# Kernel optimization log

Hardware: AMD Instinct MI355X
Metric: run time of the kernel (lower is better)

## Reference

```python
import jax, jax.numpy as jnp
import numpy as np

D_STATE = 16
D_CONV = 4


def _ln_cf(x, w, b, eps=1e-6):
    # channels_first LayerNorm over dim 1 of (B,C,H,W)
    u = x.mean(1, keepdims=True)
    s = ((x - u) ** 2).mean(1, keepdims=True)
    return w[:, None, None] * ((x - u) / jnp.sqrt(s + eps)) + b[:, None, None]


def _ln_last(x, w, b, eps=1e-5):
    u = x.mean(-1, keepdims=True)
    s = ((x - u) ** 2).mean(-1, keepdims=True)
    return (x - u) / jnp.sqrt(s + eps) * w + b


def _mamba(xn, Win, convw, convb, Wx, Wdt, bdt, Alog, Dp):
    # xn: (B, L, d_model); returns (B, L, d_inner) (out_proj is Identity in this module)
    B, L, _ = xn.shape
    di = Win.shape[0] // 2
    xz = xn @ Win.T                                   # (B,L,2*di), in_proj bias=False
    xc, z = xz[..., :di], xz[..., di:]
    # causal depthwise conv1d along L (pad left d_conv-1, slice == torch pad+trim)
    xt = jnp.pad(xc.transpose(0, 2, 1), ((0, 0), (0, 0), (D_CONV - 1, 0)))
    xt = jax.lax.conv_general_dilated(xt, convw[:, None, :], (1,), 'VALID',
                                      dimension_numbers=('NCH', 'OIH', 'NCH'),
                                      feature_group_count=di)
    xs = jax.nn.silu(xt + convb[None, :, None]).transpose(0, 2, 1)  # (B,L,di)
    dtr = Wdt.shape[1]
    x_dbl = xs @ Wx.T                                 # (B,L,dtr+2*ds)
    dt = x_dbl[..., :dtr]
    Bm = x_dbl[..., dtr:dtr + D_STATE]                # (B,L,ds)
    Cm = x_dbl[..., dtr + D_STATE:]                   # (B,L,ds)
    delta = jax.nn.softplus(dt @ Wdt.T + bdt)         # (B,L,di)
    A = -jnp.exp(Alog)                                # (di,ds)
    dA = jnp.exp(delta[..., None] * A)                # (B,L,di,ds)
    dBx = delta[..., None] * Bm[:, :, None, :] * xs[..., None]

    def step(h, ab):
        a, b2 = ab
        h = a * h + b2
        return h, h

    h0 = jnp.zeros((B, di, D_STATE), xn.dtype)
    _, hs = jax.lax.scan(step, h0, (dA.transpose(1, 0, 2, 3), dBx.transpose(1, 0, 2, 3)))
    y = jnp.einsum('lbds,bls->bld', hs, Cm) + xs * Dp
    return y * jax.nn.silu(z)


def _dwconv2d(u, k, dil):
    c = k.shape[0]
    return jax.lax.conv_general_dilated(u, k[:, None], (1, 1),
                                        [(dil, dil), (dil, dil)],
                                        rhs_dilation=(dil, dil),
                                        dimension_numbers=('NCHW', 'OIHW', 'NCHW'),
                                        feature_group_count=c)


def _block(x, gamma1, gamma2, ln1_w, ln1_b, mn_w, mn_b,
           f_Win, f_convw, f_convb, f_Wx, f_Wdt, f_bdt, f_Alog, f_D,
           b_Win, b_convw, b_convb, b_Wx, b_Wdt, b_bdt, b_Alog, b_D,
           Wout, msff_win, msff_dw1, msff_dw2, msff_dw3, msff_wout):
    B, C, H, W = x.shape
    L = H * W
    # --- BiPixelMambaLayer branch ---
    x1 = _ln_cf(x, ln1_w, ln1_b)                       # norm1 (channels_first)
    xf = x1.reshape(B, C, L).transpose(0, 2, 1)        # (B,L,C)
    xn = _ln_last(xf, mn_w, mn_b)                      # inner nn.LayerNorm (eps=1e-5)
    yf = _mamba(xn, f_Win, f_convw, f_convb, f_Wx, f_Wdt, f_bdt, f_Alog, f_D)
    yb = _mamba(xn[:, ::-1], b_Win, b_convw, b_convb, b_Wx, b_Wdt, b_bdt, b_Alog, b_D)
    yo = (yf + yb[:, ::-1]) @ Wout.T                   # shared out_proj (bias=False)
    x = x + gamma1[:, None, None] * (yo.transpose(0, 2, 1).reshape(B, C, H, W) + x1)
    # --- MSFF branch (norm1 reused) ---
    inp = x
    xm = _ln_cf(x, ln1_w, ln1_b)
    h = jnp.einsum('oc,bchw->bohw', msff_win, xm)      # project_in (1x1x1 conv, depth=1)
    hid = msff_dw1.shape[0]
    h1 = _dwconv2d(h[:, :hid], msff_dw1, 1)            # Conv3d 3x3x3 w/ depth=1 == 2D center slice
    h2 = _dwconv2d(h[:, hid:2 * hid], msff_dw2, 2)
    h3 = _dwconv2d(h[:, 2 * hid:], msff_dw3, 3)
    g = jax.nn.gelu(h1, approximate=False) * h2 * h3
    xm = jnp.einsum('oc,bchw->bohw', msff_wout, g)     # project_out
    return inp + gamma2[:, None, None] * xm


def setup_inputs() -> dict:
    key = jax.random.key(0)
    ks = jax.random.split(key, 40)
    dim, di, dtr, ds, hid, Bn, H, W = 96, 192, 6, 16, 192, 2, 64, 64
    r = lambda i, shape, s=0.05: jax.random.normal(ks[i], shape, jnp.float32) * s
    inp = {
        'x': r(0, (Bn, dim, H, W), 1.0),
        'gamma1': r(1, (dim,), 0.1), 'gamma2': r(2, (dim,), 0.1),
        'ln1_w': 1.0 + r(3, (dim,), 0.1), 'ln1_b': r(4, (dim,), 0.1),
        'mn_w': 1.0 + r(5, (dim,), 0.1), 'mn_b': r(6, (dim,), 0.1),
    }
    i = 7
    for p in ('f_', 'b_'):
        inp[p + 'Win'] = r(i, (2 * di, dim)); i += 1
        inp[p + 'convw'] = r(i, (di, D_CONV), 0.2); i += 1
        inp[p + 'convb'] = r(i, (di,), 0.1); i += 1
        inp[p + 'Wx'] = r(i, (dtr + 2 * ds, di)); i += 1
        inp[p + 'Wdt'] = r(i, (di, dtr), 0.1); i += 1
        inp[p + 'bdt'] = r(i, (di,), 0.1); i += 1
        inp[p + 'Alog'] = jax.random.uniform(ks[i], (di, ds), jnp.float32, 0.0, 2.5); i += 1
        inp[p + 'D'] = r(i, (di,), 0.5); i += 1
    inp['Wout'] = r(i, (dim, di)); i += 1
    inp['msff_win'] = r(i, (3 * hid, dim)); i += 1
    inp['msff_dw1'] = r(i, (hid, 3, 3), 0.2); i += 1
    inp['msff_dw2'] = r(i, (hid, 3, 3), 0.2); i += 1
    inp['msff_dw3'] = r(i, (hid, 3, 3), 0.2); i += 1
    inp['msff_wout'] = r(i, (dim, hid)); i += 1
    return inp


def reference(x, gamma1, gamma2, ln1_w, ln1_b, mn_w, mn_b,
              f_Win, f_convw, f_convb, f_Wx, f_Wdt, f_bdt, f_Alog, f_D,
              b_Win, b_convw, b_convb, b_Wx, b_Wdt, b_bdt, b_Alog, b_D,
              Wout, msff_win, msff_dw1, msff_dw2, msff_dw3, msff_wout):
    return _block(x, gamma1, gamma2, ln1_w, ln1_b, mn_w, mn_b,
                  f_Win, f_convw, f_convb, f_Wx, f_Wdt, f_bdt, f_Alog, f_D,
                  b_Win, b_convw, b_convb, b_Wx, b_Wdt, b_bdt, b_Alog, b_D,
                  Wout, msff_win, msff_dw1, msff_dw2, msff_dw3, msff_wout)
```

## Files before the change

kernel.cpp:

```cpp
#include <hip/hip_runtime.h>
#include <hip/hip_bf16.h>
#include <math.h>

typedef __hip_bfloat16 bf16;
typedef _Float16 f16;
typedef f16  f16x8  __attribute__((ext_vector_type(8)));
typedef short short8 __attribute__((ext_vector_type(8)));
typedef unsigned short ushort8 __attribute__((ext_vector_type(8)));
typedef float floatx4 __attribute__((ext_vector_type(4)));

#define L_SEQ 4096
#define BATCH 2
#define DIM   96
#define DI    192
#define DS    16
#define HID   192
#define NPOS  (BATCH * L_SEQ)
#define NCH   256
#define CHUNK 16
#define GRP   16
#define NGRP  (NCH / GRP)
#define NREC  (2 * BATCH * DI)
#define LDBL  40
#define PLANE (4 * NCH * DI * 8)
#define LOG2E 1.44269504088896f
#define TP    32

__device__ __forceinline__ float silu_f(float x) { return x / (1.f + __expf(-x)); }
__device__ __forceinline__ float softplus_f(float x) {
    return fmaxf(x, 0.f) + __logf(1.f + __expf(-fabsf(x)));
}
__device__ __forceinline__ float b2f(bf16 v) { return __bfloat162float(v); }
__device__ __forceinline__ float us2f(unsigned short u) {
    union { unsigned int i; float f; } cv; cv.i = ((unsigned int)u) << 16; return cv.f;
}
__device__ __forceinline__ short f2bs(float v) {
    bf16 t = __float2bfloat16(v); return *(short*)&t;
}

__global__ void k_ln_inproj_prep(const float* __restrict__ x,
                                 const float* __restrict__ ln1w, const float* __restrict__ ln1b,
                                 const float* __restrict__ mnw,  const float* __restrict__ mnb,
                                 const float* __restrict__ fWin, const float* __restrict__ bWin,
                                 bf16* __restrict__ XZF, bf16* __restrict__ XZB,
                                 const float* __restrict__ fWx,  const float* __restrict__ bWx,
                                 const float* __restrict__ Wout, const float* __restrict__ mwin,
                                 const float* __restrict__ mwout,
                                 const float* __restrict__ fAlog, const float* __restrict__ bAlog,
                                 const float* __restrict__ mdw1, const float* __restrict__ mdw2,
                                 const float* __restrict__ mdw3,
                                 bf16* __restrict__ war, float* __restrict__ a2tab,
                                 float* __restrict__ mdwt) {
    __shared__ float xt[DIM][TP + 1];
    __shared__ float rs[8][TP], rss[8][TP];
    __shared__ float uu[TP], rr[TP];
    __shared__ __align__(16) unsigned short xnt[TP][104];
    if (blockIdx.x >= NPOS / TP) {
        int i = (blockIdx.x - NPOS / TP) * 256 + threadIdx.x;
        if (i < 106752) {
            float v;
            if (i < 7296)        v = fWx[i];
            else if (i < 14592)  v = bWx[i - 7296];
            else if (i < 33024)  v = Wout[i - 14592];
            else if (i < 88320)  v = mwin[i - 33024];
            else                 v = mwout[i - 88320];
            war[i] = __float2bfloat16(v);
        } else if (i < 112896) {
            int j = i - 106752;
            int dirq = j / 3072, rem = j % 3072;
            const float* al = dirq ? bAlog : fAlog;
            a2tab[j] = -__expf(al[rem]) * LOG2E;
        } else if (i < 118080) {
            int j = i - 112896;
            int cv = j / 1728, rem = j % 1728;
            int tap = rem / 192, c = rem % 192;
            const float* src = (cv == 0) ? mdw1 : (cv == 1) ? mdw2 : mdw3;
            mdwt[j] = src[c * 9 + tap];
        }
        return;
    }
    int p0 = blockIdx.x * TP;
    int b = p0 >> 12, l0 = p0 & (L_SEQ - 1);
    int t = threadIdx.x;
    int tg = t >> 5, li = t & 31;

    for (int idx = t; idx < DIM * TP; idx += 256) {
        int c = idx >> 5, q = idx & 31;
        xt[c][q] = x[((size_t)(b * DIM + c)) * L_SEQ + l0 + q];
    }
    __syncthreads();
    {
        float s = 0.f, ss = 0.f;
        for (int c = tg; c < DIM; c += 8) { float v = xt[c][li]; s += v; ss += v * v; }
        rs[tg][li] = s; rss[tg][li] = ss;
    }
    __syncthreads();
    if (t < TP) {
        float s = 0.f, ss = 0.f;
#pragma unroll
        for (int g = 0; g < 8; g++) { s += rs[g][t]; ss += rss[g][t]; }
        float u = s / DIM;
        uu[t] = u; rr[t] = rsqrtf(ss / DIM - u * u + 1e-6f);
    }
    __syncthreads();
    {
        float u = uu[li], r = rr[li];
        float s2 = 0.f, ss2 = 0.f;
        for (int c = tg; c < DIM; c += 8) {
            float tv = ln1w[c] * (xt[c][li] - u) * r + ln1b[c];
            xt[c][li] = tv;
            s2 += tv; ss2 += tv * tv;
        }
        rs[tg][li] = s2; rss[tg][li] = ss2;
    }
    __syncthreads();
    if (t < TP) {
        float s = 0.f, ss = 0.f;
#pragma unroll
        for (int g = 0; g < 8; g++) { s += rs[g][t]; ss += rss[g][t]; }
        float u = s / DIM;
        uu[t] = u; rr[t] = rsqrtf(ss / DIM - u * u + 1e-5f);
    }
    __syncthreads();
    for (int idx = t; idx < DIM * TP; idx += 256) {
        int q = idx / DIM, c = idx % DIM;
        bf16 tv = __float2bfloat16((xt[c][q] - uu[q]) * rr[q] * mnw[c] + mnb[c]);
        xnt[q][c] = *(unsigned short*)&tv;
    }
    __syncthreads();
    int w = t >> 6, lane = t & 63;
    int lm = lane & 15, quad = lane >> 4;
    int mh = w & 1, nbase = (w >> 1) * 192;
    short8 a[3];
    const unsigned short* xr = &xnt[mh * 16 + lm][0];
#pragma unroll
    for (int k = 0; k < 3; k++)
        a[k] = *(const short8*)(xr + k * 32 + quad * 8);
#pragma unroll
    for (int dir = 0; dir < 2; dir++) {
        const float* W = dir ? bWin : fWin;
        bf16* XZ = dir ? XZB : XZF;
        floatx4 acc[12];
#pragma unroll
        for (int tt = 0; tt < 12; tt++) acc[tt] = (floatx4){0.f, 0.f, 0.f, 0.f};
#pragma unroll
        for (int k = 0; k < 3; k++) {
            int k0 = k * 32 + quad * 8;
#pragma unroll
            for (int tt = 0; tt < 12; tt++) {
                int n = nbase + tt * 16 + lm;
                const float* wp = W + n * 96 + k0;
                float4 w0 = *(const float4*)wp;
                float4 w1 = *(const float4*)(wp + 4);
                short8 bq;
                bq[0] = f2bs(w0.x); bq[1] = f2bs(w0.y); bq[2] = f2bs(w0.z); bq[3] = f2bs(w0.w);
                bq[4] = f2bs(w1.x); bq[5] = f2bs(w1.y); bq[6] = f2bs(w1.z); bq[7] = f2bs(w1.w);
                acc[tt] = __builtin_amdgcn_mfma_f32_16x16x32_bf16(a[k], bq, acc[tt], 0, 0, 0);
            }
        }
#pragma unroll
        for (int tt = 0; tt < 12; tt++) {
            int n = nbase + tt * 16 + lm;
#pragma unroll
            for (int r = 0; r < 4; r++) {
                int m = p0 + mh * 16 + quad * 4 + r;
                XZ[(size_t)m * 384 + n] = __float2bfloat16(acc[tt][r]);
            }
        }
    }
}

__global__ void k_conv_dbl(const bf16* __restrict__ XZF, const bf16* __restrict__ XZB,
                           const float* __restrict__ fw, const float* __restrict__ fb,
                           const float* __restrict__ bw, const float* __restrict__ bb,
                           const bf16* __restrict__ fWxB, const bf16* __restrict__ bWxB,
                           float* __restrict__ DBLF, float* __restrict__ DBLB,
                           bf16* __restrict__ XSF, bf16* __restrict__ XSB) {
    __shared__ __align__(16) unsigned short xs_t[64][200];
    int dirb = blockIdx.y;
    int p0 = blockIdx.x * 64;
    const bf16* XZ = dirb ? XZB : XZF;
    const float* cw = dirb ? bw : fw;
    const float* cb = dirb ? bb : fb;
    bf16* XS = dirb ? XSB : XSF;

    for (int u = threadIdx.x; u < 64 * 24; u += 256) {
        int dg = u % 24, pl = u / 24;
        int p = p0 + pl;
        int b = p >> 12, l = p & (L_SEQ - 1);
        int d0 = dg * 8;
        float4 w[8];
#pragma unroll
        for (int j = 0; j < 8; j++) w[j] = *(const float4*)(cw + (d0 + j) * 4);
        float acc[8];
#pragma unroll
        for (int j = 0; j < 8; j++) acc[j] = cb[d0 + j];
#pragma unroll
        for (int k = 0; k < 4; k++) {
            int ls = dirb ? (l + 3 - k) : (l - 3 + k);
            if (ls >= 0 && ls < L_SEQ) {
                ushort8 xv = *(const ushort8*)((const unsigned short*)XZ +
                               ((size_t)(b * L_SEQ + ls)) * 384 + d0);
#pragma unroll
                for (int j = 0; j < 8; j++) {
                    float wk = (k == 0) ? w[j].x : (k == 1) ? w[j].y : (k == 2) ? w[j].z : w[j].w;
                    acc[j] += wk * us2f(xv[j]);
                }
            }
        }
        ushort8 ov;
#pragma unroll
        for (int j = 0; j < 8; j++) {
            bf16 tv = __float2bfloat16(silu_f(acc[j]));
            ov[j] = *(unsigned short*)&tv;
        }
        *(ushort8*)((unsigned short*)XS + (size_t)p * DI + d0) = ov;
        *(ushort8*)&xs_t[pl][d0] = ov;
    }
    __syncthreads();
    int t = threadIdx.x;
    int w = t >> 6, lane = t & 63;
    int lm = lane & 15, quad = lane >> 4;
    const bf16* Wx = dirb ? bWxB : fWxB;
    float* DBL = dirb ? DBLB : DBLF;
    floatx4 acc[3];
#pragma unroll
    for (int tt = 0; tt < 3; tt++) acc[tt] = (floatx4){0.f, 0.f, 0.f, 0.f};
    const unsigned short* ar = &xs_t[w * 16 + lm][0];
#pragma unroll
    for (int k = 0; k < 6; k++) {
        int k0 = k * 32 + quad * 8;
        short8 a = *(const short8*)(ar + k0);
#pragma unroll
        for (int tt = 0; tt < 3; tt++) {
            int n = tt * 16 + lm;
            short8 bq = (n < 38) ? *(const short8*)((const short*)Wx + n * 192 + k0)
                                 : (short8){0,0,0,0,0,0,0,0};
            acc[tt] = __builtin_amdgcn_mfma_f32_16x16x32_bf16(a, bq, acc[tt], 0, 0, 0);
        }
    }
#pragma unroll
    for (int tt = 0; tt < 3; tt++) {
        int n = tt * 16 + lm;
        if (n < 38) {
            int nn = (n >= 6) ? n + 2 : n;
#pragma unroll
            for (int r = 0; r < 4; r++) {
                int m = p0 + w * 16 + quad * 4 + r;
                DBL[(size_t)m * LDBL + nn] = acc[tt][r];
            }
        }
    }
}

__global__ void k_scan_p1g(const float* __restrict__ DBLF, const float* __restrict__ DBLB,
                           const bf16* __restrict__ XSF,  const bf16* __restrict__ XSB,
                           const float* __restrict__ fWdt, const float* __restrict__ fbdt,
                           const float* __restrict__ bWdt, const float* __restrict__ bbdt,
                           const float* __restrict__ a2tab,
                           f16* __restrict__ Pexc, f16* __restrict__ Qexc,
                           float* __restrict__ Pg, float* __restrict__ Qg) {
    __shared__ f16x8 Pl[2][GRP][16];
    __shared__ f16x8 Ql[2][GRP][16];
    int dsl = blockIdx.x, grp = blockIdx.y, dirb = blockIdx.z;
    int t = threadIdx.x;
    int chunk = t >> 4, dl = t & 15;
    int d = dsl * 16 + dl;
    int b = dirb & 1, dir = dirb >> 1;
    int gc = grp * GRP + chunk;

    const float* DBL = dir ? DBLB : DBLF;
    const bf16*  XS  = dir ? XSB  : XSF;
    const float* wdt = (dir ? bWdt : fWdt) + d * 6;
    float bdtv = (dir ? bbdt : fbdt)[d];

    float wd[6];
#pragma unroll
    for (int r = 0; r < 6; r++) wd[r] = wdt[r];
    const float* a2p = a2tab + (dir * DI + d) * 16;
    float A2[16], h[16];
#pragma unroll
    for (int v = 0; v < 4; v++) {
        float4 a2v = *(const float4*)(a2p + 4 * v);
        A2[4*v] = a2v.x; A2[4*v+1] = a2v.y; A2[4*v+2] = a2v.z; A2[4*v+3] = a2v.w;
    }
#pragma unroll
    for (int s = 0; s < 16; s++) h[s] = 0.f;

    int l = dir ? (L_SEQ - 1 - gc * CHUNK) : gc * CHUNK;
    int stp = dir ? -1 : 1;
    float sumdel = 0.f;

    for (int i = 0; i < CHUNK; i++) {
        size_t p = (size_t)b * L_SEQ + l;
        const float* row = DBL + p * LDBL;
        float dtv = bdtv;
#pragma unroll
        for (int r = 0; r < 6; r++) dtv += row[r] * wd[r];
        float del = softplus_f(dtv);
        float xs  = b2f(XS[p * DI + d]);
        const float4* bm = (const float4*)(row + 8);
        float4 B0 = bm[0], B1 = bm[1], B2 = bm[2], B3 = bm[3];
        float Bm[16] = {B0.x,B0.y,B0.z,B0.w, B1.x,B1.y,B1.z,B1.w,
                        B2.x,B2.y,B2.z,B2.w, B3.x,B3.y,B3.z,B3.w};
        float dx = del * xs;
        sumdel += del;
#pragma unroll
        for (int s = 0; s < 16; s++) {
            float dA = exp2f(del * A2[s]);
            h[s] = dA * h[s] + dx * Bm[s];
        }
        l += stp;
    }
    {
        f16x8 p0, p1, q0, q1;
#pragma unroll
        for (int j = 0; j < 8; j++) {
            q0[j] = (f16)h[j];
            q1[j] = (f16)h[8 + j];
            p0[j] = (f16)exp2f(A2[j] * sumdel);
            p1[j] = (f16)exp2f(A2[8 + j] * sumdel);
        }
        Pl[0][chunk][dl] = p0; Pl[1][chunk][dl] = p1;
        Ql[0][chunk][dl] = q0; Ql[1][chunk][dl] = q1;
    }
    __syncthreads();

    {
        int s  = t & 15, dl2 = t >> 4;
        int s8 = s >> 3, sl = s & 7;
        f16* Pp = (f16*)&Pl[s8][0][dl2];
        f16* Qp = (f16*)&Ql[s8][0][dl2];
        float runP = 1.f, runQ = 0.f;
#pragma unroll
        for (int c = 0; c < GRP; c++) {
            float pv = (float)Pp[c * 128 + sl];
            float qv = (float)Qp[c * 128 + sl];
            Pp[c * 128 + sl] = (f16)runP;
            Qp[c * 128 + sl] = (f16)runQ;
            runQ = pv * runQ + qv;
            runP *= pv;
        }
        int d2 = dsl * 16 + dl2;
        size_t gidx = (((size_t)(dirb * NGRP + grp)) * DI + d2) * 16 + s;
        Pg[gidx] = runP;
        Qg[gidx] = runQ;
    }
    __syncthreads();

    {
        size_t base = ((size_t)(dirb * NCH + gc) * DI + d) * 8;
        *(f16x8*)(Pexc + base)         = Pl[0][chunk][dl];
        *(f16x8*)(Pexc + PLANE + base) = Pl[1][chunk][dl];
        *(f16x8*)(Qexc + base)         = Ql[0][chunk][dl];
        *(f16x8*)(Qexc + PLANE + base) = Ql[1][chunk][dl];
    }
}

__global__ void k_scan_p3g(const float* __restrict__ DBLF, const float* __restrict__ DBLB,
                           const bf16* __restrict__ XSF,  const bf16* __restrict__ XSB,
                           const bf16* __restrict__ XZF,  const bf16* __restrict__ XZB,
                           const float* __restrict__ fWdt, const float* __restrict__ fbdt,
                           const float* __restrict__ bWdt, const float* __restrict__ bbdt,
                           const float* __restrict__ a2tab,
                           const float* __restrict__ fD,    const float* __restrict__ bD,
                           const f16* __restrict__ Pexc, const f16* __restrict__ Qexc,
                           const float* __restrict__ Pg, const float* __restrict__ Qg,
                           bf16* __restrict__ YSF, bf16* __restrict__ YSB) {
    __shared__ float qx[16][17];
    int dsl = blockIdx.x, grp = blockIdx.y, dirb = blockIdx.z;
    int t = threadIdx.x;
    {
        int dl = t >> 4, s = t & 15;
        int d2 = dsl * 16 + dl;
        float runQ = 0.f;
        for (int g = 0; g < grp; g++) {
            size_t i = (((size_t)(dirb * NGRP + g)) * DI + d2) * 16 + s;
            runQ = Pg[i] * runQ + Qg[i];
        }
        qx[dl][s] = runQ;
    }
    __syncthreads();

    int chunk = t >> 4, dl = t & 15;
    int d = dsl * 16 + dl;
    int gc = grp * GRP + chunk;
    int b = dirb & 1, dir = dirb >> 1;

    const float* DBL = dir ? DBLB : DBLF;
    const bf16*  XS  = dir ? XSB  : XSF;
    const bf16*  XZ  = dir ? XZB  : XZF;
    const float* wdt = (dir ? bWdt : fWdt) + d * 6;
    float bdtv = (dir ? bbdt : fbdt)[d];
    float Dp = dir ? bD[d] : fD[d];
    bf16* Y = dir ? YSB : YSF;

    float wd[6];
#pragma unroll
    for (int r = 0; r < 6; r++) wd[r] = wdt[r];
    const float* a2p = a2tab + (dir * DI + d) * 16;
    float A2[16], h[16];
#pragma unroll
    for (int v = 0; v < 4; v++) {
        float4 a2v = *(const float4*)(a2p + 4 * v);
        A2[4*v] = a2v.x; A2[4*v+1] = a2v.y; A2[4*v+2] = a2v.z; A2[4*v+3] = a2v.w;
    }
    {
        size_t base = ((size_t)(dirb * NCH + gc) * DI + d) * 8;
        f16x8 pe0 = *(const f16x8*)(Pexc + base);
        f16x8 pe1 = *(const f16x8*)(Pexc + PLANE + base);
        f16x8 qe0 = *(const f16x8*)(Qexc + base);
        f16x8 qe1 = *(const f16x8*)(Qexc + PLANE + base);
#pragma unroll
        for (int j = 0; j < 8; j++) {
            h[j]     = (float)pe0[j] * qx[dl][j]     + (float)qe0[j];
            h[8 + j] = (float)pe1[j] * qx[dl][8 + j] + (float)qe1[j];
        }
    }

    int l = dir ? (L_SEQ - 1 - gc * CHUNK) : gc * CHUNK;
    int stp = dir ? -1 : 1;

    for (int i = 0; i < CHUNK; i++) {
        size_t p = (size_t)b * L_SEQ + l;
        const float* row = DBL + p * LDBL;
        float dtv = bdtv;
#pragma unroll
        for (int r = 0; r < 6; r++) dtv += row[r] * wd[r];
        float del = softplus_f(dtv);
        float xs  = b2f(XS[p * DI + d]);
        float z   = b2f(XZ[p * 384 + 192 + d]);
        const float4* bm = (const float4*)(row + 8);
        float4 B0 = bm[0], B1 = bm[1], B2 = bm[2], B3 = bm[3];
        float4 C0 = bm[4], C1 = bm[5], C2 = bm[6], C3 = bm[7];
        float Bm[16] = {B0.x,B0.y,B0.z,B0.w, B1.x,B1.y,B1.z,B1.w,
                        B2.x,B2.y,B2.z,B2.w, B3.x,B3.y,B3.z,B3.w};
        float Cm[16] = {C0.x,C0.y,C0.z,C0.w, C1.x,C1.y,C1.z,C1.w,
                        C2.x,C2.y,C2.z,C2.w, C3.x,C3.y,C3.z,C3.w};
        float dx = del * xs;
        float pr = 0.f;
#pragma unroll
        for (int s = 0; s < 16; s++) {
            float dA = exp2f(del * A2[s]);
            h[s] = dA * h[s] + dx * Bm[s];
            pr += h[s] * Cm[s];
        }
        Y[p * DI + d] = __float2bfloat16((pr + xs * Dp) * silu_f(z));
        l += stp;
    }
}

__global__ void k_out_mid(const bf16* __restrict__ Y1, const bf16* __restrict__ Y2,
                          const bf16* __restrict__ W,
                          const float* __restrict__ x, const float* __restrict__ gamma1,
                          const float* __restrict__ ln1w, const float* __restrict__ ln1b,
                          float* __restrict__ XMID, bf16* __restrict__ XM2cl) {
    __shared__ float yt[DIM][TP + 1];
    __shared__ float xt[DIM][TP + 1];
    __shared__ float rs[8][TP], rss[8][TP];
    __shared__ float uu[TP], rr[TP];
    int p0 = blockIdx.x * TP;
    int b = p0 >> 12, l0 = p0 & (L_SEQ - 1);
    int t = threadIdx.x;
    int tg = t >> 5, li = t & 31;

    {
        int w = t >> 6, lane = t & 63;
        int lm = lane & 15, quad = lane >> 4;
        int mh = w & 1, nb = (w >> 1) * 3;
        const short* A1p = (const short*)Y1 + (size_t)(p0 + mh * 16 + lm) * 192 + quad * 8;
        const short* A2p = (const short*)Y2 + (size_t)(p0 + mh * 16 + lm) * 192 + quad * 8;
        const short* Wp  = (const short*)W;
        floatx4 acc[3];
#pragma unroll
        for (int tt = 0; tt < 3; tt++) acc[tt] = (floatx4){0.f, 0.f, 0.f, 0.f};
#pragma unroll
        for (int k = 0; k < 6; k++) {
            int k0 = k * 32;
            short8 a1 = *(const short8*)(A1p + k0);
            short8 a2 = *(const short8*)(A2p + k0);
#pragma unroll
            for (int tt = 0; tt < 3; tt++) {
                int n = (nb + tt) * 16 + lm;
                short8 bq = *(const short8*)(Wp + (size_t)n * 192 + k0 + quad * 8);
                acc[tt] = __builtin_amdgcn_mfma_f32_16x16x32_bf16(a1, bq, acc[tt], 0, 0, 0);
                acc[tt] = __builtin_amdgcn_mfma_f32_16x16x32_bf16(a2, bq, acc[tt], 0, 0, 0);
            }
        }
#pragma unroll
        for (int tt = 0; tt < 3; tt++) {
            int c = (nb + tt) * 16 + lm;
#pragma unroll
            for (int r = 0; r < 4; r++)
                yt[c][mh * 16 + quad * 4 + r] = acc[tt][r];
        }
    }
    for (int idx = t; idx < DIM * TP; idx += 256) {
        int c = idx >> 5, q = idx & 31;
        xt[c][q] = x[((size_t)(b * DIM + c)) * L_SEQ + l0 + q];
    }
    __syncthreads();
    {
        float s = 0.f, ss = 0.f;
        for (int c = tg; c < DIM; c += 8) { float v = xt[c][li]; s += v; ss += v * v; }
        rs[tg][li] = s; rss[tg][li] = ss;
    }
    __syncthreads();
    if (t < TP) {
        float s = 0.f, ss = 0.f;
#pragma unroll
        for (int g = 0; g < 8; g++) { s += rs[g][t]; ss += rss[g][t]; }
        float u = s / DIM;
        uu[t] = u; rr[t] = rsqrtf(ss / DIM - u * u + 1e-6f);
    }
    __syncthreads();
    {
        float u = uu[li], r = rr[li];
        float s = 0.f, ss = 0.f;
        for (int c = tg; c < DIM; c += 8) {
            float xv = xt[c][li];
            float x1 = ln1w[c] * (xv - u) * r + ln1b[c];
            float v = xv + gamma1[c] * (yt[c][li] + x1);
            XMID[((size_t)(b * DIM + c)) * L_SEQ + l0 + li] = v;
            xt[c][li] = v;
            s += v; ss += v * v;
        }
        rs[tg][li] = s; rss[tg][li] = ss;
    }
    __syncthreads();
    if (t < TP) {
        float s = 0.f, ss = 0.f;
#pragma unroll
        for (int g = 0; g < 8; g++) { s += rs[g][t]; ss += rss[g][t]; }
        float u = s / DIM;
        uu[t] = u; rr[t] = rsqrtf(ss / DIM - u * u + 1e-6f);
    }
    __syncthreads();
    for (int idx = t; idx < DIM * TP; idx += 256) {
        int q = idx / DIM, c = idx % DIM;
        XM2cl[(size_t)(p0 + q) * DIM + c] =
            __float2bfloat16(ln1w[c] * (xt[c][q] - uu[q]) * rr[q] + ln1b[c]);
    }
}

__global__ void mfma_nt(const bf16* __restrict__ A, const bf16* __restrict__ W,
                        bf16* __restrict__ C, int M, int N, int K, int ldc) {
    int wave = threadIdx.x >> 6, lane = threadIdx.x & 63;
    int m0 = blockIdx.x * 64 + wave * 16;
    int n0 = blockIdx.y * 64;
    int lm = lane & 15, quad = lane >> 4;
    const short* Ap = (const short*)A + (size_t)(m0 + lm) * K + quad * 8;
    const short* Wp = (const short*)W;
    floatx4 acc[4];
#pragma unroll
    for (int t = 0; t < 4; t++) acc[t] = (floatx4){0.f, 0.f, 0.f, 0.f};
    for (int k0 = 0; k0 < K; k0 += 32) {
        short8 a = *(const short8*)(Ap + k0);
#pragma unroll
        for (int t = 0; t < 4; t++) {
            int n = n0 + t * 16 + lm;
            short8 b = (n < N) ? *(const short8*)(Wp + (size_t)n * K + k0 + quad * 8)
                               : (short8){0,0,0,0,0,0,0,0};
            acc[t] = __builtin_amdgcn_mfma_f32_16x16x32_bf16(a, b, acc[t], 0, 0, 0);
        }
    }
#pragma unroll
    for (int t = 0; t < 4; t++) {
        int n = n0 + t * 16 + lm;
        if (n < N) {
#pragma unroll
            for (int r = 0; r < 4; r++) {
                int m = m0 + quad * 4 + r;
                C[(size_t)m * ldc + n] = __float2bfloat16(acc[t][r]);
            }
        }
    }
}

__global__ void k_msff_outres(const bf16* __restrict__ H, const float* __restrict__ mdwt,
                              const bf16* __restrict__ mwoutB,
                              const float* __restrict__ XMID, const float* __restrict__ gamma2,
                              float* __restrict__ out) {
    __shared__ __align__(16) unsigned short gt[32][200];
    int p0 = blockIdx.x * 32;
    int t = threadIdx.x;
    const unsigned short* Hu = (const unsigned short*)H;

    for (int u = t; u < 32 * 24; u += 256) {
        int cg = u % 24, pl = u / 24;
        int p = p0 + pl;
        int c0 = cg * 8;
        int b = p >> 12, l = p & (L_SEQ - 1);
        int y = l >> 6, xc = l & 63;
        float a1[8] = {}, a2[8] = {}, a3[8] = {};
#pragma unroll
        for (int ky = 0; ky < 3; ky++) {
#pragma unroll
            for (int kx = 0; kx < 3; kx++) {
                int tap = ky * 3 + kx;
                {
                    int y1 = y + (ky - 1), x1 = xc + (kx - 1);
                    if (y1 >= 0 && y1 < 64 && x1 >= 0 && x1 < 64) {
                        float4 w0 = *(const float4*)(mdwt + tap * 192 + c0);
                        float4 w1 = *(const float4*)(mdwt + tap * 192 + c0 + 4);
                        ushort8 hv = *(const ushort8*)(Hu +
                            ((size_t)(b * L_SEQ + y1 * 64 + x1)) * 576 + c0);
                        float wv[8] = {w0.x,w0.y,w0.z,w0.w, w1.x,w1.y,w1.z,w1.w};
#pragma unroll
                        for (int j = 0; j < 8; j++) a1[j] += wv[j] * us2f(hv[j]);
                    }
                }
                {
                    int y2 = y + (ky - 1) * 2, x2 = xc + (kx - 1) * 2;
                    if (y2 >= 0 && y2 < 64 && x2 >= 0 && x2 < 64) {
                        float4 w0 = *(const float4*)(mdwt + (9 + tap) * 192 + c0);
                        float4 w1 = *(const float4*)(mdwt + (9 + tap) * 192 + c0 + 4);
                        ushort8 hv = *(const ushort8*)(Hu +
                            ((size_t)(b * L_SEQ + y2 * 64 + x2)) * 576 + 192 + c0);
                        float wv[8] = {w0.x,w0.y,w0.z,w0.w, w1.x,w1.y,w1.z,w1.w};
#pragma unroll
                        for (int j = 0; j < 8; j++) a2[j] += wv[j] * us2f(hv[j]);
                    }
                }
                {
                    int y3 = y + (ky - 1) * 3, x3 = xc + (kx - 1) * 3;
                    if (y3 >= 0 && y3 < 64 && x3 >= 0 && x3 < 64) {
                        float4 w0 = *(const float4*)(mdwt + (18 + tap) * 192 + c0);
                        float4 w1 = *(const float4*)(mdwt + (18 + tap) * 192 + c0 + 4);
                        ushort8 hv = *(const ushort8*)(Hu +
                            ((size_t)(b * L_SEQ + y3 * 64 + x3)) * 576 + 384 + c0);
                        float wv[8] = {w0.x,w0.y,w0.z,w0.w, w1.x,w1.y,w1.z,w1.w};
#pragma unroll
                        for (int j = 0; j < 8; j++) a3[j] += wv[j] * us2f(hv[j]);
                    }
                }
            }
        }
        ushort8 ov;
#pragma unroll
        for (int j = 0; j < 8; j++) {
            float ge = 0.5f * a1[j] * (1.f + erff(a1[j] * 0.70710678118f));
            bf16 tv = __float2bfloat16(ge * a2[j] * a3[j]);
            ov[j] = *(unsigned short*)&tv;
        }
        *(ushort8*)&gt[pl][c0] = ov;
    }
    __syncthreads();
    int w = t >> 6, lane = t & 63;
    int lm = lane & 15, quad = lane >> 4;
    int nt = w & 1, mb = (w >> 1) * 3;
    floatx4 acc[3];
#pragma unroll
    for (int tt = 0; tt < 3; tt++) acc[tt] = (floatx4){0.f, 0.f, 0.f, 0.f};
    const unsigned short* br = &gt[nt * 16 + lm][0];
#pragma unroll
    for (int k = 0; k < 6; k++) {
        int k0 = k * 32 + quad * 8;
        short8 bq = *(const short8*)(br + k0);
#pragma unroll
        for (int tt = 0; tt < 3; tt++) {
            int m = (mb + tt) * 16 + lm;
            short8 a = *(const short8*)((const short*)mwoutB + m * 192 + k0);
            acc[tt] = __builtin_amdgcn_mfma_f32_16x16x32_bf16(a, bq, acc[tt], 0, 0, 0);
        }
    }
    int b = p0 >> 12, l0 = p0 & (L_SEQ - 1);
#pragma unroll
    for (int tt = 0; tt < 3; tt++) {
#pragma unroll
        for (int r = 0; r < 4; r++) {
            int m = (mb + tt) * 16 + quad * 4 + r;
            size_t idx = ((size_t)(b * DIM + m)) * L_SEQ + l0 + nt * 16 + lm;
            out[idx] = XMID[idx] + gamma2[m] * acc[tt][r];
        }
    }
}

extern "C" void kernel_launch(void* const* d_in, const int* in_sizes, int n_in,
                              void* d_out, int out_size, void* d_ws, size_t ws_size,
                              hipStream_t stream) {
    const float* x      = (const float*)d_in[0];
    const float* gamma1 = (const float*)d_in[1];
    const float* gamma2 = (const float*)d_in[2];
    const float* ln1w   = (const float*)d_in[3];
    const float* ln1b   = (const float*)d_in[4];
    const float* mnw    = (const float*)d_in[5];
    const float* mnb    = (const float*)d_in[6];
    const float* fWin   = (const float*)d_in[7];
    const float* fconvw = (const float*)d_in[8];
    const float* fconvb = (const float*)d_in[9];
    const float* fWx    = (const float*)d_in[10];
    const float* fWdt   = (const float*)d_in[11];
    const float* fbdt   = (const float*)d_in[12];
    const float* fAlog  = (const float*)d_in[13];
    const float* fD     = (const float*)d_in[14];
    const float* bWin   = (const float*)d_in[15];
    const float* bconvw = (const float*)d_in[16];
    const float* bconvb = (const float*)d_in[17];
    const float* bWx    = (const float*)d_in[18];
    const float* bWdt   = (const float*)d_in[19];
    const float* bbdt   = (const float*)d_in[20];
    const float* bAlog  = (const float*)d_in[21];
    const float* bD     = (const float*)d_in[22];
    const float* Wout   = (const float*)d_in[23];
    const float* mwin   = (const float*)d_in[24];
    const float* mdw1   = (const float*)d_in[25];
    const float* mdw2   = (const float*)d_in[26];
    const float* mdw3   = (const float*)d_in[27];
    const float* mwout  = (const float*)d_in[28];
    float* out = (float*)d_out;

    float* ws = (float*)d_ws;
    bf16*  XZF   = (bf16*)(ws + 393216);
    bf16*  XZB   = (bf16*)(ws + 1966080);
    bf16*  XSF   = (bf16*)(ws + 3538944);
    bf16*  XSB   = (bf16*)(ws + 4325376);
    float* DBLF  = ws + 5111808;
    float* DBLB  = ws + 5439488;
    f16*   Ph    = (f16*)(ws + 5767168);
    f16*   Qh    = (f16*)(ws + 8912896);
    bf16*  YSFbf = (bf16*)(ws + 12058624);
    bf16*  YSBbf = (bf16*)(ws + 12845056);
    float* XMID  = ws + 14417920;
    bf16*  XM2cl = (bf16*)(ws + 15204352);
    bf16*  Hcl   = (bf16*)(ws + 15597568);
    bf16*  WAR   = (bf16*)(ws + 18743296);
    float* A2tab = ws + 18833536;
    float* MDWT  = ws + 18839680;
    float* Pgb   = ws + 18844864;
    float* Qgb   = ws + 19041472;

    const bf16* fWxB   = WAR;
    const bf16* bWxB   = WAR + 7296;
    const bf16* WoutB  = WAR + 14592;
    const bf16* mwinB  = WAR + 33024;
    const bf16* mwoutB = WAR + 88320;

    k_ln_inproj_prep<<<NPOS / TP + 462, 256, 0, stream>>>(
        x, ln1w, ln1b, mnw, mnb, fWin, bWin, XZF, XZB,
        fWx, bWx, Wout, mwin, mwout, fAlog, bAlog, mdw1, mdw2, mdw3,
        WAR, A2tab, MDWT);
    k_conv_dbl<<<dim3(NPOS / 64, 2), 256, 0, stream>>>(
        XZF, XZB, fconvw, fconvb, bconvw, bconvb,
        fWxB, bWxB, DBLF, DBLB, XSF, XSB);
    k_scan_p1g<<<dim3(DI / 16, NGRP, 4), 256, 0, stream>>>(
        DBLF, DBLB, XSF, XSB, fWdt, fbdt, bWdt, bbdt,
        A2tab, Ph, Qh, Pgb, Qgb);
    k_scan_p3g<<<dim3(DI / 16, NGRP, 4), 256, 0, stream>>>(
        DBLF, DBLB, XSF, XSB, XZF, XZB,
        fWdt, fbdt, bWdt, bbdt, A2tab, fD, bD,
        Ph, Qh, Pgb, Qgb, YSFbf, YSBbf);
    k_out_mid<<<NPOS / TP, 256, 0, stream>>>(
        YSFbf, YSBbf, WoutB, x, gamma1, ln1w, ln1b, XMID, XM2cl);
    mfma_nt<<<dim3(128, 9), 256, 0, stream>>>(XM2cl, mwinB, Hcl, NPOS, 576, DIM, 576);
    k_msff_outres<<<NPOS / 32, 256, 0, stream>>>(Hcl, MDWT, mwoutB, XMID, gamma2, out);
}
```

Measured before the change: 279.4 us.

## Split LayerNorm from in_proj GEMM and pre-convert Win weights to bf16

The fused LayerNorm + in_proj kernel is split in two. The prep kernel now writes normalized activations to global memory as bf16 and also converts fWin/bWin to bf16 alongside the other weights. A new generic MFMA GEMM kernel then computes both directions' in_proj over a wider grid. This removes the per-tile fp32-to-bf16 weight conversion and the low-occupancy 12-accumulator loop, at the cost of an extra global round-trip for the normalized input and one more launch. The new GEMM's pad6 and float-output options are unused here.

```diff
diff --git a/kernel.cpp b/kernel.cpp
--- a/kernel.cpp
+++ b/kernel.cpp
@@ -34,44 +34,42 @@
 __device__ __forceinline__ float us2f(unsigned short u) {
     union { unsigned int i; float f; } cv; cv.i = ((unsigned int)u) << 16; return cv.f;
 }
-__device__ __forceinline__ short f2bs(float v) {
-    bf16 t = __float2bfloat16(v); return *(short*)&t;
-}
-
-__global__ void k_ln_inproj_prep(const float* __restrict__ x,
-                                 const float* __restrict__ ln1w, const float* __restrict__ ln1b,
-                                 const float* __restrict__ mnw,  const float* __restrict__ mnb,
-                                 const float* __restrict__ fWin, const float* __restrict__ bWin,
-                                 bf16* __restrict__ XZF, bf16* __restrict__ XZB,
-                                 const float* __restrict__ fWx,  const float* __restrict__ bWx,
-                                 const float* __restrict__ Wout, const float* __restrict__ mwin,
-                                 const float* __restrict__ mwout,
-                                 const float* __restrict__ fAlog, const float* __restrict__ bAlog,
-                                 const float* __restrict__ mdw1, const float* __restrict__ mdw2,
-                                 const float* __restrict__ mdw3,
-                                 bf16* __restrict__ war, float* __restrict__ a2tab,
-                                 float* __restrict__ mdwt) {
+
+__global__ void k_ln12_prep(const float* __restrict__ x,
+                            const float* __restrict__ ln1w, const float* __restrict__ ln1b,
+                            const float* __restrict__ mnw,  const float* __restrict__ mnb,
+                            bf16* __restrict__ XNbf,
+                            const float* __restrict__ fWin, const float* __restrict__ bWin,
+                            const float* __restrict__ fWx,  const float* __restrict__ bWx,
+                            const float* __restrict__ Wout, const float* __restrict__ mwin,
+                            const float* __restrict__ mwout,
+                            const float* __restrict__ fAlog, const float* __restrict__ bAlog,
+                            const float* __restrict__ mdw1, const float* __restrict__ mdw2,
+                            const float* __restrict__ mdw3,
+                            bf16* __restrict__ war, float* __restrict__ a2tab,
+                            float* __restrict__ mdwt) {
     __shared__ float xt[DIM][TP + 1];
     __shared__ float rs[8][TP], rss[8][TP];
     __shared__ float uu[TP], rr[TP];
-    __shared__ __align__(16) unsigned short xnt[TP][104];
     if (blockIdx.x >= NPOS / TP) {
         int i = (blockIdx.x - NPOS / TP) * 256 + threadIdx.x;
-        if (i < 106752) {
+        if (i < 180480) {
             float v;
-            if (i < 7296)        v = fWx[i];
-            else if (i < 14592)  v = bWx[i - 7296];
-            else if (i < 33024)  v = Wout[i - 14592];
-            else if (i < 88320)  v = mwin[i - 33024];
-            else                 v = mwout[i - 88320];
+            if (i < 36864)        v = fWin[i];
+            else if (i < 73728)   v = bWin[i - 36864];
+            else if (i < 81024)   v = fWx[i - 73728];
+            else if (i < 88320)   v = bWx[i - 81024];
+            else if (i < 106752)  v = Wout[i - 88320];
+            else if (i < 162048)  v = mwin[i - 106752];
+            else                  v = mwout[i - 162048];
             war[i] = __float2bfloat16(v);
-        } else if (i < 112896) {
-            int j = i - 106752;
+        } else if (i < 186624) {
+            int j = i - 180480;
             int dirq = j / 3072, rem = j % 3072;
             const float* al = dirq ? bAlog : fAlog;
             a2tab[j] = -__expf(al[rem]) * LOG2E;
-        } else if (i < 118080) {
-            int j = i - 112896;
+        } else if (i < 191808) {
+            int j = i - 186624;
             int cv = j / 1728, rem = j % 1728;
             int tap = rem / 192, c = rem % 192;
             const float* src = (cv == 0) ? mdw1 : (cv == 1) ? mdw2 : mdw3;
@@ -124,47 +122,48 @@
     __syncthreads();
     for (int idx = t; idx < DIM * TP; idx += 256) {
         int q = idx / DIM, c = idx % DIM;
-        bf16 tv = __float2bfloat16((xt[c][q] - uu[q]) * rr[q] * mnw[c] + mnb[c]);
-        xnt[q][c] = *(unsigned short*)&tv;
-    }
-    __syncthreads();
-    int w = t >> 6, lane = t & 63;
+        XNbf[(size_t)(p0 + q) * DIM + c] =
+            __float2bfloat16((xt[c][q] - uu[q]) * rr[q] * mnw[c] + mnb[c]);
+    }
+}
+
+__global__ void mfma_nt_dir(const bf16* __restrict__ A0, const bf16* __restrict__ A1,
+                            const bf16* __restrict__ W0, const bf16* __restrict__ W1,
+                            void* __restrict__ C0, void* __restrict__ C1,
+                            int M, int N, int K, int ldc, int pad6, int obf) {
+    int z = blockIdx.z;
+    const bf16* A = z ? A1 : A0;
+    const bf16* W = z ? W1 : W0;
+    void* C = z ? C1 : C0;
+    int wave = threadIdx.x >> 6, lane = threadIdx.x & 63;
+    int m0 = blockIdx.x * 64 + wave * 16;
+    int n0 = blockIdx.y * 64;
     int lm = lane & 15, quad = lane >> 4;
-    int mh = w & 1, nbase = (w >> 1) * 192;
-    short8 a[3];
-    const unsigned short* xr = &xnt[mh * 16 + lm][0];
-#pragma unroll
-    for (int k = 0; k < 3; k++)
-        a[k] = *(const short8*)(xr + k * 32 + quad * 8);
-#pragma unroll
-    for (int dir = 0; dir < 2; dir++) {
-        const float* W = dir ? bWin : fWin;
-        bf16* XZ = dir ? XZB : XZF;
-        floatx4 acc[12];
-#pragma unroll
-        for (int tt = 0; tt < 12; tt++) acc[tt] = (floatx4){0.f, 0.f, 0.f, 0.f};
-#pragma unroll
-        for (int k = 0; k < 3; k++) {
-            int k0 = k * 32 + quad * 8;
-#pragma unroll
-            for (int tt = 0; tt < 12; tt++) {
-                int n = nbase + tt * 16 + lm;
-                const float* wp = W + n * 96 + k0;
-                float4 w0 = *(const float4*)wp;
-                float4 w1 = *(const float4*)(wp + 4);
-                short8 bq;
-                bq[0] = f2bs(w0.x); bq[1] = f2bs(w0.y); bq[2] = f2bs(w0.z); bq[3] = f2bs(w0.w);
-                bq[4] = f2bs(w1.x); bq[5] = f2bs(w1.y); bq[6] = f2bs(w1.z); bq[7] = f2bs(w1.w);
-                acc[tt] = __builtin_amdgcn_mfma_f32_16x16x32_bf16(a[k], bq, acc[tt], 0, 0, 0);
-            }
-        }
-#pragma unroll
-        for (int tt = 0; tt < 12; tt++) {
-            int n = nbase + tt * 16 + lm;
+    const short* Ap = (const short*)A + (size_t)(m0 + lm) * K + quad * 8;
+    const short* Wp = (const short*)W;
+    floatx4 acc[4];
+#pragma unroll
+    for (int t = 0; t < 4; t++) acc[t] = (floatx4){0.f, 0.f, 0.f, 0.f};
+    for (int k0 = 0; k0 < K; k0 += 32) {
+        short8 a = *(const short8*)(Ap + k0);
+#pragma unroll
+        for (int t = 0; t < 4; t++) {
+            int n = n0 + t * 16 + lm;
+            short8 b = (n < N) ? *(const short8*)(Wp + (size_t)n * K + k0 + quad * 8)
+                               : (short8){0,0,0,0,0,0,0,0};
+            acc[t] = __builtin_amdgcn_mfma_f32_16x16x32_bf16(a, b, acc[t], 0, 0, 0);
+        }
+    }
+#pragma unroll
+    for (int t = 0; t < 4; t++) {
+        int n = n0 + t * 16 + lm;
+        if (n < N) {
+            int nn = (pad6 && n >= 6) ? n + 2 : n;
 #pragma unroll
             for (int r = 0; r < 4; r++) {
-                int m = p0 + mh * 16 + quad * 4 + r;
-                XZ[(size_t)m * 384 + n] = __float2bfloat16(acc[tt][r]);
+                int m = m0 + quad * 4 + r;
+                if (obf) ((bf16*)C)[(size_t)m * ldc + nn] = __float2bfloat16(acc[t][r]);
+                else     ((float*)C)[(size_t)m * ldc + nn] = acc[t][r];
             }
         }
     }
@@ -711,6 +710,7 @@
     float* out = (float*)d_out;
 
     float* ws = (float*)d_ws;
+    bf16*  XNbf  = (bf16*)(ws);
     bf16*  XZF   = (bf16*)(ws + 393216);
     bf16*  XZB   = (bf16*)(ws + 1966080);
     bf16*  XSF   = (bf16*)(ws + 3538944);
@@ -730,16 +730,20 @@
     float* Pgb   = ws + 18844864;
     float* Qgb   = ws + 19041472;
 
-    const bf16* fWxB   = WAR;
-    const bf16* bWxB   = WAR + 7296;
-    const bf16* WoutB  = WAR + 14592;
-    const bf16* mwinB  = WAR + 33024;
-    const bf16* mwoutB = WAR + 88320;
-
-    k_ln_inproj_prep<<<NPOS / TP + 462, 256, 0, stream>>>(
-        x, ln1w, ln1b, mnw, mnb, fWin, bWin, XZF, XZB,
-        fWx, bWx, Wout, mwin, mwout, fAlog, bAlog, mdw1, mdw2, mdw3,
-        WAR, A2tab, MDWT);
+    const bf16* fWinB  = WAR;
+    const bf16* bWinB  = WAR + 36864;
+    const bf16* fWxB   = WAR + 73728;
+    const bf16* bWxB   = WAR + 81024;
+    const bf16* WoutB  = WAR + 88320;
+    const bf16* mwinB  = WAR + 106752;
+    const bf16* mwoutB = WAR + 162048;
+
+    k_ln12_prep<<<NPOS / TP + 750, 256, 0, stream>>>(
+        x, ln1w, ln1b, mnw, mnb, XNbf,
+        fWin, bWin, fWx, bWx, Wout, mwin, mwout,
+        fAlog, bAlog, mdw1, mdw2, mdw3, WAR, A2tab, MDWT);
+    mfma_nt_dir<<<dim3(128, 6, 2), 256, 0, stream>>>(XNbf, XNbf, fWinB, bWinB,
+                                                     XZF, XZB, NPOS, 384, DIM, 384, 0, 1);
     k_conv_dbl<<<dim3(NPOS / 64, 2), 256, 0, stream>>>(
         XZF, XZB, fconvw, fconvb, bconvw, bconvb,
         fWxB, bWxB, DBLF, DBLB, XSF, XSB);
```

Result: faster. 269.1 us (-3.7%).
